# Optimization experiments

Measured on AMD Instinct MI355X. Metric: run time of the kernel, lower is better.

Reference implementation:

```python
import jax, jax.numpy as jnp
import numpy as np

N_NODES = 50000   # num_hpo
N_EDGES = 100000  # hyperedges
NNZ = 1000000     # incidences
HID = 128


def setup_inputs() -> dict:
    key = jax.random.key(0)
    k1, k2, k3, k4, k5, k6 = jax.random.split(key, 6)
    rows = jax.random.randint(k1, (NNZ,), 0, N_NODES)
    cols = jax.random.randint(k2, (NNZ,), 0, N_EDGES)
    vals = jax.random.uniform(k3, (NNZ,), dtype=jnp.float32)
    X0 = jax.random.normal(k4, (N_NODES, HID), dtype=jnp.float32) * 0.01
    W0 = jax.random.normal(k5, (HID, HID), dtype=jnp.float32) * (1.0 / np.sqrt(HID))
    W1 = jax.random.normal(k6, (HID, HID), dtype=jnp.float32) * (1.0 / np.sqrt(HID))
    return {"rows": rows, "cols": cols, "vals": vals, "X0": X0, "W0": W0,
            "W1": W1, "num_hpo": N_NODES, "num_edges": N_EDGES}


def _propagate(rows, cols, vals, X, num_hpo, num_edges):
    # degree of hyperedges (column sums) and nodes (row sums)
    d_e = jnp.clip(jax.ops.segment_sum(vals, cols, num_segments=num_edges), 1e-6, None)
    d_v = jnp.clip(jax.ops.segment_sum(vals, rows, num_segments=num_hpo), 1e-6, None)
    dv_inv_sqrt = d_v ** -0.5          # [N]
    de_inv = 1.0 / d_e                 # [E]
    Y = dv_inv_sqrt[:, None] * X       # [N, d]
    # H^T @ Y : scatter node rows into hyperedge buckets
    Ye = jax.ops.segment_sum(vals[:, None] * Y[rows], cols, num_segments=num_edges)  # [E, d]
    Ye = de_inv[:, None] * Ye
    # H @ Ye : scatter hyperedge rows back to nodes
    Yn = jax.ops.segment_sum(vals[:, None] * Ye[cols], rows, num_segments=num_hpo)   # [N, d]
    return dv_inv_sqrt[:, None] * Yn


def reference(rows, cols, vals, X0, W0, W1, num_hpo, num_edges):
    # layer 0: relu(theta0(P @ X0)); nn.Linear(bias=False) => X @ W.T
    X1 = jax.nn.relu(_propagate(rows, cols, vals, X0, num_hpo, num_edges) @ W0.T)
    # layer 1: theta1(P @ X1)
    Z = _propagate(rows, cols, vals, X1, num_hpo, num_edges) @ W1.T
    return Z
```

## Files before the change

kernel.cpp:

```cpp
#include <hip/hip_runtime.h>
#include <hip/hip_fp16.h>
#include <math.h>

#define NNODES 50000
#define NEDGES 100000
#define HID 128
#define NKEYS (NEDGES + NNODES)

#define NB_E ((NEDGES + 255) >> 8)
#define NB_N ((NNODES + 255) >> 8)
#define NB (NB_E + NB_N)
#define CAP_E 3072
#define CAP_N 6144
#define PART_CHUNK 8192

__device__ __forceinline__ int region_start(int b) {
  return (b < NB_E) ? b * CAP_E : NB_E * CAP_E + (b - NB_E) * CAP_N;
}

__global__ __launch_bounds__(256) void partition_kernel(
    const int* __restrict__ rows, const int* __restrict__ cols,
    const float* __restrict__ vals, int* __restrict__ bucket_cur,
    int2* __restrict__ bkt_items, int nnz) {
  __shared__ int cnt[NB];
  __shared__ int wbase[NB];
  for (int k = threadIdx.x; k < NB; k += 256) cnt[k] = 0;
  __syncthreads();
  int start = blockIdx.x * PART_CHUNK;
  int end = start + PART_CHUNK;
  if (end > nnz) end = nnz;
  for (int i = start + threadIdx.x; i < end; i += 256) {
    atomicAdd(&cnt[cols[i] >> 8], 1);
    atomicAdd(&cnt[NB_E + (rows[i] >> 8)], 1);
  }
  __syncthreads();
  for (int k = threadIdx.x; k < NB; k += 256) {
    int c = cnt[k];
    wbase[k] = c ? region_start(k) + atomicAdd(&bucket_cur[k], c) : 0;
    cnt[k] = 0;
  }
  __syncthreads();
  for (int i = start + threadIdx.x; i < end; i += 256) {
    int c = cols[i], r = rows[i];
    int v = __float_as_int(vals[i]);
    int be = c >> 8;
    int p = wbase[be] + atomicAdd(&cnt[be], 1);
    bkt_items[p] = make_int2(((c & 255) << 18) | r, v);
    int bn = NB_E + (r >> 8);
    int q = wbase[bn] + atomicAdd(&cnt[bn], 1);
    bkt_items[q] = make_int2(((r & 255) << 18) | c, v);
  }
}

__global__ __launch_bounds__(1024) void bucket_scan_kernel(
    const int* __restrict__ bucket_cur, int* __restrict__ bucket_base) {
  int t = threadIdx.x;
  int lane = t & 63, wid = t >> 6;
  int x = (t < NB) ? bucket_cur[t] : 0;
  int incl = x;
#pragma unroll
  for (int d = 1; d < 64; d <<= 1) {
    int tt = __shfl_up(incl, d, 64);
    if (lane >= d) incl += tt;
  }
  __shared__ int ws[16];
  if (lane == 63) ws[wid] = incl;
  __syncthreads();
  int woff = 0;
  for (int k = 0; k < wid; ++k) woff += ws[k];
  int excl = woff + incl - x;
  if (t < NB) bucket_base[t] = excl;
  if (t == NB - 1) bucket_base[NB] = excl + x;
}

__global__ __launch_bounds__(256) void place_kernel(
    const int* __restrict__ bucket_base, const int* __restrict__ bucket_cur,
    const int2* __restrict__ bkt_items, int* __restrict__ off,
    int2* __restrict__ pair, float* __restrict__ dein,
    float* __restrict__ dvis) {
  int b = blockIdx.x;
  int rs = region_start(b);
  int cntb = bucket_cur[b];
  int s = bucket_base[b];
  __shared__ int kcnt[256];
  __shared__ float ksum[256];
  __shared__ int kbase[256];
  __shared__ int ws[4];
  int t = threadIdx.x;
  kcnt[t] = 0;
  ksum[t] = 0.f;
  __syncthreads();
  for (int j = rs + t; j < rs + cntb; j += 256) {
    int2 it = bkt_items[j];
    int k = it.x >> 18;
    atomicAdd(&kcnt[k], 1);
    atomicAdd(&ksum[k], __int_as_float(it.y));
  }
  __syncthreads();
  int x = kcnt[t];
  int lane = t & 63, wid = t >> 6;
  int incl = x;
#pragma unroll
  for (int d = 1; d < 64; d <<= 1) {
    int tt = __shfl_up(incl, d, 64);
    if (lane >= d) incl += tt;
  }
  if (lane == 63) ws[wid] = incl;
  __syncthreads();
  int woff = 0;
  for (int k = 0; k < wid; ++k) woff += ws[k];
  int excl = woff + incl - x;
  kbase[t] = s + excl;
  float sum = fmaxf(ksum[t], 1e-6f);
  if (b < NB_E) {
    int kglob = (b << 8) | t;
    if (kglob < NEDGES) {
      off[kglob] = s + excl;
      dein[kglob] = 1.0f / sum;
    }
  } else {
    int kglob = ((b - NB_E) << 8) | t;
    if (kglob < NNODES) {
      off[NEDGES + kglob] = s + excl;
      dvis[kglob] = rsqrtf(sum);
    }
  }
  if (b == NB - 1 && t == 0) off[NKEYS] = s + cntb;
  __syncthreads();
  kcnt[t] = 0;
  __syncthreads();
  for (int j = rs + t; j < rs + cntb; j += 256) {
    int2 it = bkt_items[j];
    int k = it.x >> 18;
    int pos = kbase[k] + atomicAdd(&kcnt[k], 1);
    pair[pos] = make_int2(it.x & 0x3FFFF, it.y);
  }
}

__global__ __launch_bounds__(256) void scalex_h_kernel(
    const float* __restrict__ X, const float* __restrict__ dvis,
    uint2* __restrict__ Yh) {
  int i = blockIdx.x * 256 + threadIdx.x;
  if (i >= NNODES * 32) return;
  float s = dvis[i >> 5];
  float4 v = reinterpret_cast<const float4*>(X)[i];
  __half2 a = __float22half2_rn(make_float2(s * v.x, s * v.y));
  __half2 b = __float22half2_rn(make_float2(s * v.z, s * v.w));
  uint2 o;
  o.x = *reinterpret_cast<unsigned*>(&a);
  o.y = *reinterpret_cast<unsigned*>(&b);
  Yh[i] = o;
}

__device__ __forceinline__ void gather_body16(
    const uint4* __restrict__ S, const int* __restrict__ off,
    const int2* __restrict__ pair, int e, int lane, float* acc) {
  int grp = lane >> 4, li = lane & 15;
  int s = off[e], t = off[e + 1];
  int d = t - s;
  int q = d >> 2, r = d & 3;
  int j = s + grp * q + (grp < r ? grp : r);
  int jend = j + q + (grp < r ? 1 : 0);
  for (; j + 1 < jend; j += 2) {
    int2 p0 = pair[j], p1 = pair[j + 1];
    float w0 = __int_as_float(p0.y), w1 = __int_as_float(p1.y);
    uint4 u0 = S[(size_t)p0.x * 16 + li];
    uint4 u1 = S[(size_t)p1.x * 16 + li];
    float2 f0 = __half22float2(*reinterpret_cast<__half2*>(&u0.x));
    float2 f1 = __half22float2(*reinterpret_cast<__half2*>(&u0.y));
    float2 f2 = __half22float2(*reinterpret_cast<__half2*>(&u0.z));
    float2 f3 = __half22float2(*reinterpret_cast<__half2*>(&u0.w));
    acc[0] = fmaf(w0, f0.x, acc[0]); acc[1] = fmaf(w0, f0.y, acc[1]);
    acc[2] = fmaf(w0, f1.x, acc[2]); acc[3] = fmaf(w0, f1.y, acc[3]);
    acc[4] = fmaf(w0, f2.x, acc[4]); acc[5] = fmaf(w0, f2.y, acc[5]);
    acc[6] = fmaf(w0, f3.x, acc[6]); acc[7] = fmaf(w0, f3.y, acc[7]);
    float2 g0 = __half22float2(*reinterpret_cast<__half2*>(&u1.x));
    float2 g1 = __half22float2(*reinterpret_cast<__half2*>(&u1.y));
    float2 g2 = __half22float2(*reinterpret_cast<__half2*>(&u1.z));
    float2 g3 = __half22float2(*reinterpret_cast<__half2*>(&u1.w));
    acc[0] = fmaf(w1, g0.x, acc[0]); acc[1] = fmaf(w1, g0.y, acc[1]);
    acc[2] = fmaf(w1, g1.x, acc[2]); acc[3] = fmaf(w1, g1.y, acc[3]);
    acc[4] = fmaf(w1, g2.x, acc[4]); acc[5] = fmaf(w1, g2.y, acc[5]);
    acc[6] = fmaf(w1, g3.x, acc[6]); acc[7] = fmaf(w1, g3.y, acc[7]);
  }
  if (j < jend) {
    int2 p0 = pair[j];
    float w0 = __int_as_float(p0.y);
    uint4 u0 = S[(size_t)p0.x * 16 + li];
    float2 f0 = __half22float2(*reinterpret_cast<__half2*>(&u0.x));
    float2 f1 = __half22float2(*reinterpret_cast<__half2*>(&u0.y));
    float2 f2 = __half22float2(*reinterpret_cast<__half2*>(&u0.z));
    float2 f3 = __half22float2(*reinterpret_cast<__half2*>(&u0.w));
    acc[0] = fmaf(w0, f0.x, acc[0]); acc[1] = fmaf(w0, f0.y, acc[1]);
    acc[2] = fmaf(w0, f1.x, acc[2]); acc[3] = fmaf(w0, f1.y, acc[3]);
    acc[4] = fmaf(w0, f2.x, acc[4]); acc[5] = fmaf(w0, f2.y, acc[5]);
    acc[6] = fmaf(w0, f3.x, acc[6]); acc[7] = fmaf(w0, f3.y, acc[7]);
  }
#pragma unroll
  for (int k = 0; k < 8; ++k) {
    acc[k] += __shfl_xor(acc[k], 16);
    acc[k] += __shfl_xor(acc[k], 32);
  }
}

__global__ __launch_bounds__(256) void gather_hh_kernel(
    const uint4* __restrict__ src, uint4* __restrict__ dst,
    const int* __restrict__ off, const int2* __restrict__ pair,
    const float* __restrict__ seg_scale, int nseg) {
  int e = blockIdx.x * 4 + (threadIdx.x >> 6);
  if (e >= nseg) return;
  int lane = threadIdx.x & 63;
  float acc[8] = {0.f, 0.f, 0.f, 0.f, 0.f, 0.f, 0.f, 0.f};
  gather_body16(src, off, pair, e, lane, acc);
  if (lane < 16) {
    float sc = seg_scale ? seg_scale[e] : 1.0f;
    __half2 h0 = __float22half2_rn(make_float2(sc * acc[0], sc * acc[1]));
    __half2 h1 = __float22half2_rn(make_float2(sc * acc[2], sc * acc[3]));
    __half2 h2 = __float22half2_rn(make_float2(sc * acc[4], sc * acc[5]));
    __half2 h3 = __float22half2_rn(make_float2(sc * acc[6], sc * acc[7]));
    uint4 o;
    o.x = *reinterpret_cast<unsigned*>(&h0);
    o.y = *reinterpret_cast<unsigned*>(&h1);
    o.z = *reinterpret_cast<unsigned*>(&h2);
    o.w = *reinterpret_cast<unsigned*>(&h3);
    dst[(size_t)e * 16 + lane] = o;
  }
}

__device__ __forceinline__ void cvt8(uint4 u, float* f) {
  float2 a = __half22float2(*reinterpret_cast<__half2*>(&u.x));
  float2 b = __half22float2(*reinterpret_cast<__half2*>(&u.y));
  float2 c = __half22float2(*reinterpret_cast<__half2*>(&u.z));
  float2 d = __half22float2(*reinterpret_cast<__half2*>(&u.w));
  f[0] = a.x; f[1] = a.y; f[2] = b.x; f[3] = b.y;
  f[4] = c.x; f[5] = c.y; f[6] = d.x; f[7] = d.y;
}

__global__ __launch_bounds__(256) void gemm_h_kernel(
    const uint4* __restrict__ Pnh, const float* __restrict__ dvis,
    const float* __restrict__ W, void* __restrict__ out_v, int mode) {
  __shared__ float WT[128 * 64];
  int t = threadIdx.x;
  int jb = blockIdx.x & 1;
  int rb = blockIdx.x >> 1;
  int j0 = jb << 6;
  {
    int K = t & 31;
    int Jb = t >> 5;
#pragma unroll
    for (int p = 0; p < 2; ++p) {
      int J = Jb + (p << 3);
      const float* Wb = W + (size_t)(j0 + 4 * J) * 128 + 4 * K;
      float4 g0 = *reinterpret_cast<const float4*>(Wb);
      float4 g1 = *reinterpret_cast<const float4*>(Wb + 128);
      float4 g2 = *reinterpret_cast<const float4*>(Wb + 256);
      float4 g3 = *reinterpret_cast<const float4*>(Wb + 384);
      const float* g0p = reinterpret_cast<const float*>(&g0);
      const float* g1p = reinterpret_cast<const float*>(&g1);
      const float* g2p = reinterpret_cast<const float*>(&g2);
      const float* g3p = reinterpret_cast<const float*>(&g3);
#pragma unroll
      for (int q = 0; q < 4; ++q) {
        int k = 4 * K + q;
        float4 hq = make_float4(g0p[q], g1p[q], g2p[q], g3p[q]);
        int slot = (J + k) & 15;
        *reinterpret_cast<float4*>(&WT[k * 64 + 4 * slot]) = hq;
      }
    }
  }
  __syncthreads();
  int u = t & 15;
  int rg = t >> 4;
  int rbase = rb * 64 + rg * 4;
  const float4* WT4 = reinterpret_cast<const float4*>(WT);
  float4 acc0 = make_float4(0.f, 0.f, 0.f, 0.f);
  float4 acc1 = acc0, acc2 = acc0, acc3 = acc0;
  int rr0 = rbase + 0; if (rr0 >= NNODES) rr0 = NNODES - 1;
  int rr1 = rbase + 1; if (rr1 >= NNODES) rr1 = NNODES - 1;
  int rr2 = rbase + 2; if (rr2 >= NNODES) rr2 = NNODES - 1;
  int rr3 = rbase + 3; if (rr3 >= NNODES) rr3 = NNODES - 1;
  const uint4* X0 = Pnh + (size_t)rr0 * 16;
  const uint4* X1 = Pnh + (size_t)rr1 * 16;
  const uint4* X2 = Pnh + (size_t)rr2 * 16;
  const uint4* X3 = Pnh + (size_t)rr3 * 16;
#pragma unroll 4
  for (int kk = 0; kk < 16; ++kk) {
    float x0f[8], x1f[8], x2f[8], x3f[8];
    cvt8(X0[kk], x0f);
    cvt8(X1[kk], x1f);
    cvt8(X2[kk], x2f);
    cvt8(X3[kk], x3f);
#pragma unroll
    for (int q = 0; q < 8; ++q) {
      int k = kk * 8 + q;
      float4 w4 = WT4[k * 16 + ((u + k) & 15)];
      acc0.x = fmaf(x0f[q], w4.x, acc0.x); acc0.y = fmaf(x0f[q], w4.y, acc0.y);
      acc0.z = fmaf(x0f[q], w4.z, acc0.z); acc0.w = fmaf(x0f[q], w4.w, acc0.w);
      acc1.x = fmaf(x1f[q], w4.x, acc1.x); acc1.y = fmaf(x1f[q], w4.y, acc1.y);
      acc1.z = fmaf(x1f[q], w4.z, acc1.z); acc1.w = fmaf(x1f[q], w4.w, acc1.w);
      acc2.x = fmaf(x2f[q], w4.x, acc2.x); acc2.y = fmaf(x2f[q], w4.y, acc2.y);
      acc2.z = fmaf(x2f[q], w4.z, acc2.z); acc2.w = fmaf(x2f[q], w4.w, acc2.w);
      acc3.x = fmaf(x3f[q], w4.x, acc3.x); acc3.y = fmaf(x3f[q], w4.y, acc3.y);
      acc3.z = fmaf(x3f[q], w4.z, acc3.z); acc3.w = fmaf(x3f[q], w4.w, acc3.w);
    }
  }
#pragma unroll
  for (int m = 0; m < 4; ++m) {
    int r = rbase + m;
    if (r >= NNODES) break;
    float4 a = (m == 0) ? acc0 : (m == 1) ? acc1 : (m == 2) ? acc2 : acc3;
    float s = dvis[r];
    float4 o = make_float4(s * a.x, s * a.y, s * a.z, s * a.w);
    if (mode == 1) {
      o.x = fmaxf(o.x, 0.f) * s; o.y = fmaxf(o.y, 0.f) * s;
      o.z = fmaxf(o.z, 0.f) * s; o.w = fmaxf(o.w, 0.f) * s;
      __half2 ha = __float22half2_rn(make_float2(o.x, o.y));
      __half2 hb = __float22half2_rn(make_float2(o.z, o.w));
      uint2 ou;
      ou.x = *reinterpret_cast<unsigned*>(&ha);
      ou.y = *reinterpret_cast<unsigned*>(&hb);
      reinterpret_cast<uint2*>(out_v)[(size_t)r * 32 + (j0 >> 2) + u] = ou;
    } else {
      *reinterpret_cast<float4*>(
          &reinterpret_cast<float*>(out_v)[(size_t)r * 128 + j0 + 4 * u]) = o;
    }
  }
}

__global__ __launch_bounds__(256) void deg_fb_kernel(
    const int* __restrict__ rows, const int* __restrict__ cols,
    const float* __restrict__ vals, float* __restrict__ dv,
    float* __restrict__ de, int nnz) {
  int i = blockIdx.x * 256 + threadIdx.x;
  if (i >= nnz) return;
  float v = vals[i];
  unsafeAtomicAdd(&dv[rows[i]], v);
  unsafeAtomicAdd(&de[cols[i]], v);
}

__global__ __launch_bounds__(256) void inv_kernel(float* __restrict__ dv,
                                                  float* __restrict__ de) {
  int i = blockIdx.x * 256 + threadIdx.x;
  if (i < NNODES) {
    dv[i] = 1.0f / sqrtf(fmaxf(dv[i], 1e-6f));
  } else if (i < NNODES + NEDGES) {
    int j = i - NNODES;
    de[j] = 1.0f / fmaxf(de[j], 1e-6f);
  }
}

__global__ __launch_bounds__(256) void scatter_edge_kernel(
    const float* __restrict__ X, float* __restrict__ Ye,
    const int* __restrict__ rows, const int* __restrict__ cols,
    const float* __restrict__ vals, const float* __restrict__ dvis, int nnz) {
  int g = (blockIdx.x * 256 + threadIdx.x) >> 5;
  int lane = threadIdx.x & 31;
  if (g >= nnz) return;
  int r = rows[g], c = cols[g];
  float s = vals[g] * dvis[r];
  float4 x = reinterpret_cast<const float4*>(X)[(size_t)r * 32 + lane];
  float* dst = Ye + (size_t)c * HID + lane * 4;
  unsafeAtomicAdd(dst + 0, s * x.x);
  unsafeAtomicAdd(dst + 1, s * x.y);
  unsafeAtomicAdd(dst + 2, s * x.z);
  unsafeAtomicAdd(dst + 3, s * x.w);
}

__global__ __launch_bounds__(256) void scatter_node_kernel(
    const float* __restrict__ Ye, float* __restrict__ Yn,
    const int* __restrict__ rows, const int* __restrict__ cols,
    const float* __restrict__ vals, const float* __restrict__ dein, int nnz) {
  int g = (blockIdx.x * 256 + threadIdx.x) >> 5;
  int lane = threadIdx.x & 31;
  if (g >= nnz) return;
  int r = rows[g], c = cols[g];
  float s = vals[g] * dein[c];
  float4 y = reinterpret_cast<const float4*>(Ye)[(size_t)c * 32 + lane];
  float* dst = Yn + (size_t)r * HID + lane * 4;
  unsafeAtomicAdd(dst + 0, s * y.x);
  unsafeAtomicAdd(dst + 1, s * y.y);
  unsafeAtomicAdd(dst + 2, s * y.z);
  unsafeAtomicAdd(dst + 3, s * y.w);
}

__global__ __launch_bounds__(256) void gemm_rm_kernel(
    const float* __restrict__ Pn, const float* __restrict__ dvis,
    const float* __restrict__ W, float* __restrict__ out, int mode) {
  __shared__ float WT[128 * 64];
  int t = threadIdx.x;
  int jb = blockIdx.x & 1;
  int rb = blockIdx.x >> 1;
  int j0 = jb << 6;
  {
    int K = t & 31;
    int Jb = t >> 5;
#pragma unroll
    for (int p = 0; p < 2; ++p) {
      int J = Jb + (p << 3);
      const float* Wb = W + (size_t)(j0 + 4 * J) * 128 + 4 * K;
      float4 g0 = *reinterpret_cast<const float4*>(Wb);
      float4 g1 = *reinterpret_cast<const float4*>(Wb + 128);
      float4 g2 = *reinterpret_cast<const float4*>(Wb + 256);
      float4 g3 = *reinterpret_cast<const float4*>(Wb + 384);
      const float* g0p = reinterpret_cast<const float*>(&g0);
      const float* g1p = reinterpret_cast<const float*>(&g1);
      const float* g2p = reinterpret_cast<const float*>(&g2);
      const float* g3p = reinterpret_cast<const float*>(&g3);
#pragma unroll
      for (int q = 0; q < 4; ++q) {
        int k = 4 * K + q;
        float4 hq = make_float4(g0p[q], g1p[q], g2p[q], g3p[q]);
        int slot = (J + k) & 15;
        *reinterpret_cast<float4*>(&WT[k * 64 + 4 * slot]) = hq;
      }
    }
  }
  __syncthreads();
  int u = t & 15;
  int rg = t >> 4;
  int rbase = rb * 64 + rg * 4;
  const float4* WT4 = reinterpret_cast<const float4*>(WT);
  float4 acc0 = make_float4(0.f, 0.f, 0.f, 0.f);
  float4 acc1 = acc0, acc2 = acc0, acc3 = acc0;
  int rr0 = rbase + 0; if (rr0 >= NNODES) rr0 = NNODES - 1;
  int rr1 = rbase + 1; if (rr1 >= NNODES) rr1 = NNODES - 1;
  int rr2 = rbase + 2; if (rr2 >= NNODES) rr2 = NNODES - 1;
  int rr3 = rbase + 3; if (rr3 >= NNODES) rr3 = NNODES - 1;
  const float4* X0 = reinterpret_cast<const float4*>(Pn + (size_t)rr0 * 128);
  const float4* X1 = reinterpret_cast<const float4*>(Pn + (size_t)rr1 * 128);
  const float4* X2 = reinterpret_cast<const float4*>(Pn + (size_t)rr2 * 128);
  const float4* X3 = reinterpret_cast<const float4*>(Pn + (size_t)rr3 * 128);
#pragma unroll 4
  for (int kk = 0; kk < 32; ++kk) {
    float4 x0 = X0[kk], x1 = X1[kk], x2 = X2[kk], x3 = X3[kk];
    const float* x0p = reinterpret_cast<const float*>(&x0);
    const float* x1p = reinterpret_cast<const float*>(&x1);
    const float* x2p = reinterpret_cast<const float*>(&x2);
    const float* x3p = reinterpret_cast<const float*>(&x3);
#pragma unroll
    for (int q = 0; q < 4; ++q) {
      int k = 4 * kk + q;
      float4 w4 = WT4[k * 16 + ((u + k) & 15)];
      acc0.x = fmaf(x0p[q], w4.x, acc0.x); acc0.y = fmaf(x0p[q], w4.y, acc0.y);
      acc0.z = fmaf(x0p[q], w4.z, acc0.z); acc0.w = fmaf(x0p[q], w4.w, acc0.w);
      acc1.x = fmaf(x1p[q], w4.x, acc1.x); acc1.y = fmaf(x1p[q], w4.y, acc1.y);
      acc1.z = fmaf(x1p[q], w4.z, acc1.z); acc1.w = fmaf(x1p[q], w4.w, acc1.w);
      acc2.x = fmaf(x2p[q], w4.x, acc2.x); acc2.y = fmaf(x2p[q], w4.y, acc2.y);
      acc2.z = fmaf(x2p[q], w4.z, acc2.z); acc2.w = fmaf(x2p[q], w4.w, acc2.w);
      acc3.x = fmaf(x3p[q], w4.x, acc3.x); acc3.y = fmaf(x3p[q], w4.y, acc3.y);
      acc3.z = fmaf(x3p[q], w4.z, acc3.z); acc3.w = fmaf(x3p[q], w4.w, acc3.w);
    }
  }
#pragma unroll
  for (int m = 0; m < 4; ++m) {
    int r = rbase + m;
    if (r >= NNODES) break;
    float4 a = (m == 0) ? acc0 : (m == 1) ? acc1 : (m == 2) ? acc2 : acc3;
    float s = dvis[r];
    float4 o = make_float4(s * a.x, s * a.y, s * a.z, s * a.w);
    if (mode == 2) {
      o.x = fmaxf(o.x, 0.f); o.y = fmaxf(o.y, 0.f);
      o.z = fmaxf(o.z, 0.f); o.w = fmaxf(o.w, 0.f);
    }
    *reinterpret_cast<float4*>(&out[(size_t)r * 128 + j0 + 4 * u]) = o;
  }
}

extern "C" void kernel_launch(void* const* d_in, const int* in_sizes, int n_in,
                              void* d_out, int out_size, void* d_ws,
                              size_t ws_size, hipStream_t stream) {
  const int* rows = (const int*)d_in[0];
  const int* cols = (const int*)d_in[1];
  const float* vals = (const float*)d_in[2];
  const float* X0 = (const float*)d_in[3];
  const float* W0 = (const float*)d_in[4];
  const float* W1 = (const float*)d_in[5];
  const int nnz = in_sizes[0];
  float* out = (float*)d_out;

  const int gemm_blocks = ((NNODES + 63) / 64) * 2;

  size_t bkt_cap = (size_t)NB_E * CAP_E + (size_t)NB_N * CAP_N;
  size_t ye_elems = (size_t)NEDGES * 64;
  size_t xh_elems = (size_t)NNODES * 64;
  size_t elems = 4 * (size_t)nnz + ye_elems + 2 * xh_elems + NNODES + NEDGES +
                 (NKEYS + 1) + NB + (NB + 1);
  size_t need = elems * 4;
  bool bkt_fits = 2 * bkt_cap <= ye_elems;

  if (ws_size >= need && bkt_fits && (size_t)2 * nnz <= bkt_cap) {
    int2* pair = (int2*)d_ws;
    uint4* Yeh = (uint4*)(pair + 2 * (size_t)nnz);
    int2* bkt_items = (int2*)Yeh;
    uint4* Xh = Yeh + (size_t)NEDGES * 16;
    uint4* Pnh = Xh + (size_t)NNODES * 16;
    float* dvis = (float*)(Pnh + (size_t)NNODES * 16);
    float* dein = dvis + NNODES;
    int* off = (int*)(dein + NEDGES);
    int* bucket_cur = off + NKEYS + 1;
    int* bucket_base = bucket_cur + NB;

    hipMemsetAsync(bucket_cur, 0, NB * sizeof(int), stream);
    partition_kernel<<<(nnz + PART_CHUNK - 1) / PART_CHUNK, 256, 0, stream>>>(
        rows, cols, vals, bucket_cur, bkt_items, nnz);
    bucket_scan_kernel<<<1, 1024, 0, stream>>>(bucket_cur, bucket_base);
    place_kernel<<<NB, 256, 0, stream>>>(bucket_base, bucket_cur, bkt_items,
                                         off, pair, dein, dvis);
    scalex_h_kernel<<<(NNODES * 32 + 255) / 256, 256, 0, stream>>>(
        X0, dvis, (uint2*)Xh);

    const int eg_blocks = (NEDGES + 3) / 4;
    const int ng_blocks = (NNODES + 3) / 4;

    gather_hh_kernel<<<eg_blocks, 256, 0, stream>>>(Xh, Yeh, off, pair, dein,
                                                    NEDGES);
    gather_hh_kernel<<<ng_blocks, 256, 0, stream>>>(Yeh, Pnh, off + NEDGES,
                                                    pair, nullptr, NNODES);
    gemm_h_kernel<<<gemm_blocks, 256, 0, stream>>>(Pnh, dvis, W0, Xh, 1);

    gather_hh_kernel<<<eg_blocks, 256, 0, stream>>>(Xh, Yeh, off, pair, dein,
                                                    NEDGES);
    gather_hh_kernel<<<ng_blocks, 256, 0, stream>>>(Yeh, Pnh, off + NEDGES,
                                                    pair, nullptr, NNODES);
    gemm_h_kernel<<<gemm_blocks, 256, 0, stream>>>(Pnh, dvis, W1, out, 0);
    return;
  }

  float* dv = (float*)d_ws;
  float* de = dv + NNODES;
  float* Ye = de + NEDGES;
  float* Pn = Ye + (size_t)NEDGES * HID;
  const int scat_blocks = (nnz + 7) / 8;

  hipMemsetAsync(dv, 0, (size_t)(NNODES + NEDGES) * sizeof(float), stream);
  deg_fb_kernel<<<(nnz + 255) / 256, 256, 0, stream>>>(rows, cols, vals, dv,
                                                       de, nnz);
  inv_kernel<<<(NNODES + NEDGES + 255) / 256, 256, 0, stream>>>(dv, de);

  hipMemsetAsync(Ye, 0, (size_t)NEDGES * HID * sizeof(float), stream);
  scatter_edge_kernel<<<scat_blocks, 256, 0, stream>>>(X0, Ye, rows, cols,
                                                       vals, dv, nnz);
  hipMemsetAsync(Pn, 0, (size_t)NNODES * HID * sizeof(float), stream);
  scatter_node_kernel<<<scat_blocks, 256, 0, stream>>>(Ye, Pn, rows, cols,
                                                       vals, de, nnz);
  gemm_rm_kernel<<<gemm_blocks, 256, 0, stream>>>(Pn, dv, W0, out, 2);

  hipMemsetAsync(Ye, 0, (size_t)NEDGES * HID * sizeof(float), stream);
  scatter_edge_kernel<<<scat_blocks, 256, 0, stream>>>(out, Ye, rows, cols,
                                                       vals, dv, nnz);
  hipMemsetAsync(Pn, 0, (size_t)NNODES * HID * sizeof(float), stream);
  scatter_node_kernel<<<scat_blocks, 256, 0, stream>>>(Ye, Pn, rows, cols,
                                                       vals, de, nnz);
  gemm_rm_kernel<<<gemm_blocks, 256, 0, stream>>>(Pn, dv, W1, out, 0);
}
```

Baseline: 306.3 us.

## Move degree sums to a segmented kernel and fold node scaling into gather

Degree sums are no longer accumulated with shared-memory float atomics inside place_kernel. A new deg_kernel sums each key's CSR segment sequentially, which also makes the result deterministic. The dv^-1/2 post-scale moves from the GEMM epilogue into the node-side gather by passing dvis instead of nullptr, relying on the scale commuting with the linear map. Separately, the partition chunk is reduced to launch more partition blocks. The cost is one extra kernel launch, an extra read pass over pair, and the assumption that the gather kernel applies its scale argument for the node pass.

Result: no change. 310.1 us (+1.2%).

```diff
diff --git a/kernel.cpp b/kernel.cpp
--- a/kernel.cpp
+++ b/kernel.cpp
@@ -12,7 +12,7 @@
 #define NB (NB_E + NB_N)
 #define CAP_E 3072
 #define CAP_N 6144
-#define PART_CHUNK 8192
+#define PART_CHUNK 2048
 
 __device__ __forceinline__ int region_start(int b) {
   return (b < NB_E) ? b * CAP_E : NB_E * CAP_E + (b - NB_E) * CAP_N;
@@ -76,26 +76,19 @@
 __global__ __launch_bounds__(256) void place_kernel(
     const int* __restrict__ bucket_base, const int* __restrict__ bucket_cur,
     const int2* __restrict__ bkt_items, int* __restrict__ off,
-    int2* __restrict__ pair, float* __restrict__ dein,
-    float* __restrict__ dvis) {
+    int2* __restrict__ pair) {
   int b = blockIdx.x;
   int rs = region_start(b);
   int cntb = bucket_cur[b];
   int s = bucket_base[b];
   __shared__ int kcnt[256];
-  __shared__ float ksum[256];
   __shared__ int kbase[256];
   __shared__ int ws[4];
   int t = threadIdx.x;
   kcnt[t] = 0;
-  ksum[t] = 0.f;
-  __syncthreads();
-  for (int j = rs + t; j < rs + cntb; j += 256) {
-    int2 it = bkt_items[j];
-    int k = it.x >> 18;
-    atomicAdd(&kcnt[k], 1);
-    atomicAdd(&ksum[k], __int_as_float(it.y));
-  }
+  __syncthreads();
+  for (int j = rs + t; j < rs + cntb; j += 256)
+    atomicAdd(&kcnt[bkt_items[j].x >> 18], 1);
   __syncthreads();
   int x = kcnt[t];
   int lane = t & 63, wid = t >> 6;
@@ -111,19 +104,12 @@
   for (int k = 0; k < wid; ++k) woff += ws[k];
   int excl = woff + incl - x;
   kbase[t] = s + excl;
-  float sum = fmaxf(ksum[t], 1e-6f);
   if (b < NB_E) {
     int kglob = (b << 8) | t;
-    if (kglob < NEDGES) {
-      off[kglob] = s + excl;
-      dein[kglob] = 1.0f / sum;
-    }
+    if (kglob < NEDGES) off[kglob] = s + excl;
   } else {
     int kglob = ((b - NB_E) << 8) | t;
-    if (kglob < NNODES) {
-      off[NEDGES + kglob] = s + excl;
-      dvis[kglob] = rsqrtf(sum);
-    }
+    if (kglob < NNODES) off[NEDGES + kglob] = s + excl;
   }
   if (b == NB - 1 && t == 0) off[NKEYS] = s + cntb;
   __syncthreads();
@@ -135,6 +121,21 @@
     int pos = kbase[k] + atomicAdd(&kcnt[k], 1);
     pair[pos] = make_int2(it.x & 0x3FFFF, it.y);
   }
+}
+
+__global__ __launch_bounds__(256) void deg_kernel(
+    const int* __restrict__ off, const int2* __restrict__ pair,
+    float* __restrict__ dein, float* __restrict__ dvis) {
+  int i = blockIdx.x * 256 + threadIdx.x;
+  if (i >= NKEYS) return;
+  int s = off[i], t = off[i + 1];
+  float sum = 0.f;
+  for (int j = s; j < t; ++j) sum += __int_as_float(pair[j].y);
+  sum = fmaxf(sum, 1e-6f);
+  if (i < NEDGES)
+    dein[i] = 1.0f / sum;
+  else
+    dvis[i - NEDGES] = rsqrtf(sum);
 }
 
 __global__ __launch_bounds__(256) void scalex_h_kernel(
@@ -309,11 +310,10 @@
     int r = rbase + m;
     if (r >= NNODES) break;
     float4 a = (m == 0) ? acc0 : (m == 1) ? acc1 : (m == 2) ? acc2 : acc3;
-    float s = dvis[r];
-    float4 o = make_float4(s * a.x, s * a.y, s * a.z, s * a.w);
     if (mode == 1) {
-      o.x = fmaxf(o.x, 0.f) * s; o.y = fmaxf(o.y, 0.f) * s;
-      o.z = fmaxf(o.z, 0.f) * s; o.w = fmaxf(o.w, 0.f) * s;
+      float s = dvis[r];
+      float4 o = make_float4(fmaxf(a.x, 0.f) * s, fmaxf(a.y, 0.f) * s,
+                             fmaxf(a.z, 0.f) * s, fmaxf(a.w, 0.f) * s);
       __half2 ha = __float22half2_rn(make_float2(o.x, o.y));
       __half2 hb = __float22half2_rn(make_float2(o.z, o.w));
       uint2 ou;
@@ -322,7 +322,7 @@
       reinterpret_cast<uint2*>(out_v)[(size_t)r * 32 + (j0 >> 2) + u] = ou;
     } else {
       *reinterpret_cast<float4*>(
-          &reinterpret_cast<float*>(out_v)[(size_t)r * 128 + j0 + 4 * u]) = o;
+          &reinterpret_cast<float*>(out_v)[(size_t)r * 128 + j0 + 4 * u]) = a;
     }
   }
 }
@@ -505,7 +505,8 @@
         rows, cols, vals, bucket_cur, bkt_items, nnz);
     bucket_scan_kernel<<<1, 1024, 0, stream>>>(bucket_cur, bucket_base);
     place_kernel<<<NB, 256, 0, stream>>>(bucket_base, bucket_cur, bkt_items,
-                                         off, pair, dein, dvis);
+                                         off, pair);
+    deg_kernel<<<(NKEYS + 255) / 256, 256, 0, stream>>>(off, pair, dein, dvis);
     scalex_h_kernel<<<(NNODES * 32 + 255) / 256, 256, 0, stream>>>(
         X0, dvis, (uint2*)Xh);
 
@@ -515,13 +516,13 @@
     gather_hh_kernel<<<eg_blocks, 256, 0, stream>>>(Xh, Yeh, off, pair, dein,
                                                     NEDGES);
     gather_hh_kernel<<<ng_blocks, 256, 0, stream>>>(Yeh, Pnh, off + NEDGES,
-                                                    pair, nullptr, NNODES);
+                                                    pair, dvis, NNODES);
     gemm_h_kernel<<<gemm_blocks, 256, 0, stream>>>(Pnh, dvis, W0, Xh, 1);
 
     gather_hh_kernel<<<eg_blocks, 256, 0, stream>>>(Xh, Yeh, off, pair, dein,
                                                     NEDGES);
     gather_hh_kernel<<<ng_blocks, 256, 0, stream>>>(Yeh, Pnh, off + NEDGES,
-                                                    pair, nullptr, NNODES);
+                                                    pair, dvis, NNODES);
     gemm_h_kernel<<<gemm_blocks, 256, 0, stream>>>(Pnh, dvis, W1, out, 0);
     return;
   }
```
